# Kernel optimization log

Measured on AMD Instinct MI355X. Metric: run time of the kernel, lower is better.

The kernel has to match this reference:

```python
import jax, jax.numpy as jnp
from jax import lax
import numpy as np

B = 8192
HID = 128
FILT = 256  # stft filter length
HOP = 128
PAD = 64
NBINS = 129  # FILT//2 + 1


def setup_inputs() -> dict:
    key = jax.random.key(0)
    ks = jax.random.split(key, 16)
    def rn(k, shape, fan_in):
        return jax.random.normal(k, shape, dtype=jnp.float32) / np.sqrt(fan_in)
    inp = {
        "audio_input": jax.random.normal(ks[0], (B, 4160), dtype=jnp.float32),
        "hidden_state": jnp.zeros((B, HID), dtype=jnp.float32),
        "cell_state": jnp.zeros((B, HID), dtype=jnp.float32),
        # STFT forward basis: [2*NBINS, 1, FILT] (real then imag banks)
        "stft_w": rn(ks[1], (2 * NBINS, 1, FILT), FILT),
        # encoder: 4 conv1d layers (out, in, k), strides 1,2,2,1, pad 1
        "enc_w1": rn(ks[2], (128, 129, 3), 129 * 3), "enc_b1": jnp.zeros((128,), jnp.float32),
        "enc_w2": rn(ks[3], (64, 128, 3), 128 * 3), "enc_b2": jnp.zeros((64,), jnp.float32),
        "enc_w3": rn(ks[4], (64, 64, 3), 64 * 3),   "enc_b3": jnp.zeros((64,), jnp.float32),
        "enc_w4": rn(ks[5], (128, 64, 3), 64 * 3),  "enc_b4": jnp.zeros((128,), jnp.float32),
        # LSTMCell (PyTorch layout): gates order i,f,g,o
        "w_ih": rn(ks[6], (4 * HID, HID), HID), "w_hh": rn(ks[7], (4 * HID, HID), HID),
        "b_ih": jnp.zeros((4 * HID,), jnp.float32), "b_hh": jnp.zeros((4 * HID,), jnp.float32),
        # output head: Linear(128 -> 1) + sigmoid
        "out_w": rn(ks[8], (1, HID), HID), "out_b": jnp.zeros((1,), jnp.float32),
    }
    return inp


def _conv1d(x, w, b, stride, pad):
    # x: [N, C_in, L], w: [C_out, C_in, k]
    y = lax.conv_general_dilated(x, w, (stride,), [(pad, pad)],
                                 dimension_numbers=("NCH", "OIH", "NCH"))
    return y + b[None, :, None]


def reference(audio_input, hidden_state, cell_state, stft_w,
              enc_w1, enc_b1, enc_w2, enc_b2, enc_w3, enc_b3, enc_w4, enc_b4,
              w_ih, w_hh, b_ih, b_hh, out_w, out_b):
    b = audio_input.shape[0]
    # chunk i with context == audio_input[:, i*512 : i*512 + 576]
    chunks = jnp.stack([audio_input[:, i * 512:i * 512 + 576] for i in range(8)], axis=0)  # [8,B,576]
    x = chunks.reshape(8 * b, 576)
    # STFT: reflect pad 64 each side, conv stride 128 -> [8B, 258, 4]
    xp = jnp.pad(x, ((0, 0), (PAD, PAD)), mode="reflect")[:, None, :]
    spec = lax.conv_general_dilated(xp, stft_w, (HOP,), "VALID",
                                    dimension_numbers=("NCH", "OIH", "NCH"))
    mag = jnp.sqrt(spec[:, :NBINS] ** 2 + spec[:, NBINS:] ** 2)  # [8B,129,4]
    # encoder conv stack: 4 -> 4 -> 2 -> 1 -> 1 frames
    h1 = jax.nn.relu(_conv1d(mag, enc_w1, enc_b1, 1, 1))
    h2 = jax.nn.relu(_conv1d(h1, enc_w2, enc_b2, 2, 1))
    h3 = jax.nn.relu(_conv1d(h2, enc_w3, enc_b3, 2, 1))
    h4 = jax.nn.relu(_conv1d(h3, enc_w4, enc_b4, 1, 1))  # [8B,128,1]
    feats = h4[:, :, 0].reshape(8, b, HID)  # [8,B,128]

    def step(carry, x_t):
        h, c = carry
        gates = x_t @ w_ih.T + b_ih + h @ w_hh.T + b_hh  # [B,4H]
        i_g, f_g, g_g, o_g = jnp.split(gates, 4, axis=-1)
        c_new = jax.nn.sigmoid(f_g) * c + jax.nn.sigmoid(i_g) * jnp.tanh(g_g)
        h_new = jax.nn.sigmoid(o_g) * jnp.tanh(c_new)
        p = jax.nn.sigmoid(h_new @ out_w.T + out_b)  # [B,1]
        return (h_new, c_new), p

    (h_fin, c_fin), probs = lax.scan(step, (hidden_state, cell_state), feats)  # probs [8,B,1]
    # final = 1 - prod_i (1 - p_i), shape [B,1,1]
    final = (1.0 - jnp.prod(1.0 - probs, axis=0))[:, :, None]
    return final, h_fin, c_fin
```

## Files before the change

kernel.cpp:

```cpp
#include <hip/hip_runtime.h>
#include <hip/hip_bf16.h>
#include <math.h>

typedef __hip_bfloat16 bf16;
typedef __attribute__((ext_vector_type(4))) float f32x4;
typedef __attribute__((ext_vector_type(8))) short short8;
typedef __attribute__((ext_vector_type(4))) short short4v;

#define BATCH   8192
#define NTOT    65536
#define NT2     131072
#define NW      262144
#define HID     128

__device__ __forceinline__ float b2f(bf16 v){ return __bfloat162float(v); }
__device__ __forceinline__ bf16  f2b(float v){ return __float2bfloat16(v); }
__device__ __forceinline__ short f2bs(float v){
  bf16 b = __float2bfloat16(v);
  return *reinterpret_cast<short*>(&b);
}
__device__ __forceinline__ float sigf(float x){ return 1.0f/(1.0f+__expf(-x)); }
__device__ __forceinline__ float tanhfast(float x){
  return 1.0f - 2.0f/(__expf(2.0f*x)+1.0f);
}

__global__ __launch_bounds__(256) void k_wcvt(
    const float* __restrict__ W, bf16* __restrict__ Wb)
{
  const int idx = blockIdx.x*256 + threadIdx.x;
  if (idx < 258*256) Wb[idx] = f2b(W[idx]);
}
__global__ __launch_bounds__(256) void k_w1cvt(
    const float* __restrict__ w1, bf16* __restrict__ w1b)
{
  const int idx = blockIdx.x*256 + threadIdx.x;
  if (idx >= 61440) return;
  const int dt = idx / 20480, rem = idx % 20480;
  const int cout = rem / 160, k = rem % 160;
  const float v = (k < 129) ? w1[(cout*129 + k)*3 + dt] : 0.f;
  w1b[idx] = f2b(v);
}
__global__ __launch_bounds__(256) void k_w2cvt(
    const float* __restrict__ w2, bf16* __restrict__ w2b)
{
  const int idx = blockIdx.x*256 + threadIdx.x;
  if (idx >= 24576) return;
  const int dt = idx >> 13, cout = (idx >> 7) & 63, k = idx & 127;
  w2b[idx] = f2b(w2[(cout*128 + k)*3 + dt]);
}
__global__ __launch_bounds__(256) void k_w34cvt(
    const float* __restrict__ w3, const float* __restrict__ w4,
    bf16* __restrict__ w3e, bf16* __restrict__ w4e)
{
  const int idx = blockIdx.x*256 + threadIdx.x;
  if (idx >= 16384) return;
  if (idx < 8192){
    const int row = idx >> 7, k = idx & 127;
    const int cin = k >> 1, t = k & 1;
    w3e[idx] = f2b(w3[(row*64 + cin)*3 + 1 + t]);
  } else {
    const int i2 = idx - 8192;
    const int row = i2 >> 6, cin = i2 & 63;
    w4e[i2] = f2b(w4[(row*64 + cin)*3 + 1]);
  }
}
__global__ __launch_bounds__(256) void k_wlcvt1(
    const float* __restrict__ whh, bf16* __restrict__ wl1)
{
  const int idx = blockIdx.x*256 + threadIdx.x;
  if (idx >= 65536) return;
  wl1[idx] = f2b(whh[idx]);
}
__global__ __launch_bounds__(256) void k_wlxcvt(
    const float* __restrict__ wih, bf16* __restrict__ wlx)
{
  const int idx = blockIdx.x*256 + threadIdx.x;
  if (idx >= 65536) return;
  wlx[idx] = f2b(wih[idx]);
}

__global__ __launch_bounds__(256) void k_stft3(
    const float* __restrict__ audio, const bf16* __restrict__ Wb,
    bf16* __restrict__ mag)
{
  __shared__ __align__(16) char ALDS[96*512];
  __shared__ __align__(16) bf16 refl[4*8*64];
  const int tid = threadIdx.x, lane = tid & 63, wq = tid >> 6;
  const int r0 = blockIdx.x * 4;
  const float* arow = audio + (size_t)(r0 + wq) * 4160;

  #pragma unroll
  for (int q = 0; q < 8; ++q){
    const int e = q*64 + lane;
    const int i = e >> 6, k = e & 63;
    refl[(wq*8 + i)*64 + k] = f2b(arow[512*i + 64 - k]);
  }

  const int kgo8 = (lane>>4)*8;
  short8 Bfrag[2][8];
  #pragma unroll
  for (int ng = 0; ng < 2; ++ng){
    const int wl = ng*16 + (lane & 15);
    const int i = wl >> 2, t = wl & 3;
    #pragma unroll
    for (int ks = 0; ks < 8; ++ks){
      const int kb = ks*32 + kgo8;
      if (t == 0 && kb < 64){
        Bfrag[ng][ks] = *(const short8*)(refl + (wq*8 + i)*64 + kb);
      } else {
        const float* src = arow + 512*i + 128*t - 64 + kb;
        const float4 v0 = *(const float4*)(src);
        const float4 v1 = *(const float4*)(src + 4);
        short8 s;
        s[0]=f2bs(v0.x); s[1]=f2bs(v0.y); s[2]=f2bs(v0.z); s[3]=f2bs(v0.w);
        s[4]=f2bs(v1.x); s[5]=f2bs(v1.y); s[6]=f2bs(v1.z); s[7]=f2bs(v1.w);
        Bfrag[ng][ks] = s;
      }
    }
  }

  const int kab = (lane>>4)*16;
  for (int pass = 0; pass < 3; ++pass){
    __syncthreads();
    for (int idx = tid; idx < 96*32; idx += 256){
      const int ar = idx >> 5;
      const int cb = (idx & 31) * 16;
      const int b3 = ar >> 5, reim = (ar >> 4) & 1, bl = ar & 15;
      int bin = pass*48 + b3*16 + bl;
      if (bin > 128) bin = 128;
      const int grow = bin + reim*129;
      int off = ar*512 + cb; off ^= ((ar&7)<<4);
      *(f32x4*)(ALDS + off) = *(const f32x4*)((const char*)Wb + grow*512 + cb);
    }
    __syncthreads();

    f32x4 accRe[3][2], accIm[3][2];
    #pragma unroll
    for (int b3 = 0; b3 < 3; ++b3)
      #pragma unroll
      for (int ng = 0; ng < 2; ++ng){
        accRe[b3][ng] = f32x4{0.f,0.f,0.f,0.f};
        accIm[b3][ng] = f32x4{0.f,0.f,0.f,0.f};
      }
    #pragma unroll
    for (int ks = 0; ks < 8; ++ks){
      #pragma unroll
      for (int b3 = 0; b3 < 3; ++b3){
        const int arRe = b3*32 + (lane & 15);
        const int arIm = arRe + 16;
        int offRe = arRe*512 + ks*64 + kab; offRe ^= ((arRe&7)<<4);
        int offIm = arIm*512 + ks*64 + kab; offIm ^= ((arIm&7)<<4);
        const short8 aRe = *(const short8*)(ALDS + offRe);
        const short8 aIm = *(const short8*)(ALDS + offIm);
        #pragma unroll
        for (int ng = 0; ng < 2; ++ng){
          accRe[b3][ng] = __builtin_amdgcn_mfma_f32_16x16x32_bf16(
              aRe, Bfrag[ng][ks], accRe[b3][ng], 0, 0, 0);
          accIm[b3][ng] = __builtin_amdgcn_mfma_f32_16x16x32_bf16(
              aIm, Bfrag[ng][ks], accIm[b3][ng], 0, 0, 0);
        }
      }
    }
    #pragma unroll
    for (int b3 = 0; b3 < 3; ++b3)
      #pragma unroll
      for (int j = 0; j < 4; ++j){
        const int bin = (pass*3 + b3)*16 + (lane>>4)*4 + j;
        if (bin <= 128){
          #pragma unroll
          for (int ng = 0; ng < 2; ++ng){
            const int wl = ng*16 + (lane & 15);
            const int i = wl >> 2, t = wl & 3;
            const float re = accRe[b3][ng][j], im = accIm[b3][ng][j];
            mag[(size_t)bin*NW + (size_t)i*32768 + (r0+wq)*4 + t] =
                f2b(sqrtf(re*re + im*im));
          }
        }
      }
  }
}

#define E1_LDS (192*320)
__global__ __launch_bounds__(256) void k_enc1_gemm(
    const bf16* __restrict__ mag, const bf16* __restrict__ w1b,
    const float* __restrict__ b1, bf16* __restrict__ h1)
{
  __shared__ __align__(16) char Bs[E1_LDS];
  const int tid = threadIdx.x, lane = tid & 63, wq = tid >> 6;
  const int n0 = blockIdx.x * 32;
  const int i  = n0 >> 13, b0 = n0 & 8191;
  const size_t colbase = (size_t)i*32768 + (size_t)b0*4;

  for (int off = tid*16; off < E1_LDS; off += 256*16)
    *(f32x4*)(Bs + off) = f32x4{0.f,0.f,0.f,0.f};
  __syncthreads();
  for (int it = tid; it < 129*64; it += 256){
    const int cin = it >> 6, seg = it & 63;
    const unsigned int pair =
        *(const unsigned int*)(mag + (size_t)cin*NW + colbase + seg*2);
    #pragma unroll
    for (int q = 0; q < 2; ++q){
      const int w = seg*2 + q;
      const int row = (w>>2)*6 + (w&3) + 1;
      int off = row*320 + cin*2; off ^= ((row&7)<<4);
      *(short*)(Bs + off) = (short)((q==0) ? (pair & 0xffff) : (pair >> 16));
    }
  }
  __syncthreads();

  const int wr = wq >> 1, wc = wq & 1;
  f32x4 acc[4][4];
  #pragma unroll
  for (int mg = 0; mg < 4; ++mg)
    #pragma unroll
    for (int ng = 0; ng < 4; ++ng) acc[mg][ng] = f32x4{0.f,0.f,0.f,0.f};

  int brow[4], acol[4];
  #pragma unroll
  for (int ng = 0; ng < 4; ++ng){
    const int w = wc*64 + ng*16 + (lane & 15);
    brow[ng] = (w>>2)*6 + (w&3);
  }
  #pragma unroll
  for (int mg = 0; mg < 4; ++mg) acol[mg] = wr*64 + mg*16 + (lane & 15);
  const int kb = (lane>>4)*16;

  for (int dt = 0; dt < 3; ++dt){
    #pragma unroll
    for (int ks = 0; ks < 5; ++ks){
      short8 afr[4], bfr[4];
      #pragma unroll
      for (int mg = 0; mg < 4; ++mg)
        afr[mg] = *(const short8*)((const char*)w1b +
            ((dt*128 + acol[mg])*160 + ks*32)*2 + kb);
      #pragma unroll
      for (int ng = 0; ng < 4; ++ng){
        const int row = brow[ng] + dt;
        int off = row*320 + ks*64 + kb; off ^= ((row&7)<<4);
        bfr[ng] = *(const short8*)(Bs + off);
      }
      #pragma unroll
      for (int mg = 0; mg < 4; ++mg)
        #pragma unroll
        for (int ng = 0; ng < 4; ++ng)
          acc[mg][ng] = __builtin_amdgcn_mfma_f32_16x16x32_bf16(
              afr[mg], bfr[ng], acc[mg][ng], 0, 0, 0);
    }
  }
  #pragma unroll
  for (int mg = 0; mg < 4; ++mg)
    #pragma unroll
    for (int j = 0; j < 4; ++j){
      const int cout = wr*64 + mg*16 + (lane>>4)*4 + j;
      const float bv = b1[cout];
      #pragma unroll
      for (int ng = 0; ng < 4; ++ng){
        const int col = wc*64 + ng*16 + (lane & 15);
        float v = acc[mg][ng][j] + bv; v = v > 0.f ? v : 0.f;
        h1[(size_t)cout*NW + colbase + col] = f2b(v);
      }
    }
}

#define E2_LDS (160*256)
__global__ __launch_bounds__(256) void k_enc2_gemm(
    const bf16* __restrict__ h1, const bf16* __restrict__ w2b,
    const float* __restrict__ b2, bf16* __restrict__ h2)
{
  __shared__ __align__(16) char Bs[E2_LDS];
  const int tid = threadIdx.x, lane = tid & 63, wq = tid >> 6;
  const int n0 = blockIdx.x * 32;
  const int i  = n0 >> 13, b0 = n0 & 8191;
  const size_t colbase = (size_t)i*32768 + (size_t)b0*4;
  const size_t col2base = (size_t)i*16384 + (size_t)b0*2;

  for (int off = tid*16; off < E2_LDS; off += 256*16)
    *(f32x4*)(Bs + off) = f32x4{0.f,0.f,0.f,0.f};
  __syncthreads();
  for (int it = tid; it < 128*64; it += 256){
    const int cin = it >> 6, seg = it & 63;
    const unsigned int pair =
        *(const unsigned int*)(h1 + (size_t)cin*NW + colbase + seg*2);
    #pragma unroll
    for (int q = 0; q < 2; ++q){
      const int w = seg*2 + q;
      const int row = (w>>2)*5 + (w&3) + 1;
      int off = row*256 + cin*2; off ^= ((row&7)<<4);
      *(short*)(Bs + off) = (short)((q==0) ? (pair & 0xffff) : (pair >> 16));
    }
  }
  __syncthreads();

  const int wr = wq >> 1, wc = wq & 1;
  f32x4 acc[2][2];
  #pragma unroll
  for (int mg = 0; mg < 2; ++mg)
    #pragma unroll
    for (int ng = 0; ng < 2; ++ng) acc[mg][ng] = f32x4{0.f,0.f,0.f,0.f};

  int brow[2], acol[2];
  #pragma unroll
  for (int ng = 0; ng < 2; ++ng){
    const int wl = wc*32 + ng*16 + (lane & 15);
    brow[ng] = (wl>>1)*5 + (wl&1)*2;
  }
  #pragma unroll
  for (int mg = 0; mg < 2; ++mg) acol[mg] = wr*32 + mg*16 + (lane & 15);
  const int kb = (lane>>4)*16;

  for (int dt = 0; dt < 3; ++dt){
    #pragma unroll
    for (int ks = 0; ks < 4; ++ks){
      short8 afr[2], bfr[2];
      #pragma unroll
      for (int mg = 0; mg < 2; ++mg)
        afr[mg] = *(const short8*)((const char*)w2b +
            ((dt*64 + acol[mg])*128 + ks*32)*2 + kb);
      #pragma unroll
      for (int ng = 0; ng < 2; ++ng){
        const int row = brow[ng] + dt;
        int off = row*256 + ks*64 + kb; off ^= ((row&7)<<4);
        bfr[ng] = *(const short8*)(Bs + off);
      }
      #pragma unroll
      for (int mg = 0; mg < 2; ++mg)
        #pragma unroll
        for (int ng = 0; ng < 2; ++ng)
          acc[mg][ng] = __builtin_amdgcn_mfma_f32_16x16x32_bf16(
              afr[mg], bfr[ng], acc[mg][ng], 0, 0, 0);
    }
  }
  #pragma unroll
  for (int mg = 0; mg < 2; ++mg)
    #pragma unroll
    for (int j = 0; j < 4; ++j){
      const int cout = wr*32 + mg*16 + (lane>>4)*4 + j;
      const float bv = b2[cout];
      #pragma unroll
      for (int ng = 0; ng < 2; ++ng){
        const int col = wc*32 + ng*16 + (lane & 15);
        float v = acc[mg][ng][j] + bv; v = v > 0.f ? v : 0.f;
        h2[(size_t)cout*NT2 + col2base + col] = f2b(v);
      }
    }
}

__global__ __launch_bounds__(256) void k_enc34(
    const bf16* __restrict__ h2, const bf16* __restrict__ w3e,
    const float* __restrict__ b3, const bf16* __restrict__ w4e,
    const float* __restrict__ b4, bf16* __restrict__ h4)
{
  __shared__ __align__(16) char B1[64*256];
  __shared__ __align__(16) char B2[64*128];
  const int tid = threadIdx.x, lane = tid & 63, wq = tid >> 6;
  const int n0 = blockIdx.x * 64;

  for (int it = tid; it < 64*64; it += 256){
    const int cin = it >> 6, nl = it & 63;
    const int n = n0 + nl, i = n >> 13, b = n & 8191;
    const unsigned int pair =
        *(const unsigned int*)(h2 + (size_t)cin*NT2 + i*16384 + 2*b);
    int off = nl*256 + cin*4; off ^= ((nl&7)<<4);
    *(unsigned int*)(B1 + off) = pair;
  }
  __syncthreads();

  const int kb = (lane>>4)*16;
  f32x4 acc1[4];
  #pragma unroll
  for (int ng = 0; ng < 4; ++ng) acc1[ng] = f32x4{0.f,0.f,0.f,0.f};
  const int ar1 = wq*16 + (lane & 15);
  #pragma unroll
  for (int ks = 0; ks < 4; ++ks){
    const short8 a = *(const short8*)((const char*)w3e + (ar1*128 + ks*32)*2 + kb);
    #pragma unroll
    for (int ng = 0; ng < 4; ++ng){
      const int row = ng*16 + (lane & 15);
      int off = row*256 + ks*64 + kb; off ^= ((row&7)<<4);
      const short8 bfr = *(const short8*)(B1 + off);
      acc1[ng] = __builtin_amdgcn_mfma_f32_16x16x32_bf16(a, bfr, acc1[ng], 0, 0, 0);
    }
  }
  #pragma unroll
  for (int j = 0; j < 4; ++j){
    const int r1 = wq*16 + (lane>>4)*4 + j;
    const float bv = b3[r1];
    #pragma unroll
    for (int ng = 0; ng < 4; ++ng){
      const int col = ng*16 + (lane & 15);
      float v = acc1[ng][j] + bv; v = v > 0.f ? v : 0.f;
      int off = col*128 + r1*2; off ^= ((col&7)<<4);
      *(short*)(B2 + off) = f2bs(v);
    }
  }
  __syncthreads();

  f32x4 acc2[2][4];
  #pragma unroll
  for (int mg = 0; mg < 2; ++mg)
    #pragma unroll
    for (int ng = 0; ng < 4; ++ng) acc2[mg][ng] = f32x4{0.f,0.f,0.f,0.f};
  #pragma unroll
  for (int ks = 0; ks < 2; ++ks){
    short8 bfr[4];
    #pragma unroll
    for (int ng = 0; ng < 4; ++ng){
      const int row = ng*16 + (lane & 15);
      int off = row*128 + ks*64 + kb; off ^= ((row&7)<<4);
      bfr[ng] = *(const short8*)(B2 + off);
    }
    #pragma unroll
    for (int mg = 0; mg < 2; ++mg){
      const int ar2 = wq*32 + mg*16 + (lane & 15);
      const short8 a = *(const short8*)((const char*)w4e + (ar2*64 + ks*32)*2 + kb);
      #pragma unroll
      for (int ng = 0; ng < 4; ++ng)
        acc2[mg][ng] = __builtin_amdgcn_mfma_f32_16x16x32_bf16(a, bfr[ng], acc2[mg][ng], 0, 0, 0);
    }
  }
  #pragma unroll
  for (int mg = 0; mg < 2; ++mg)
    #pragma unroll
    for (int j = 0; j < 4; ++j){
      const int cout = wq*32 + mg*16 + (lane>>4)*4 + j;
      const float bv = b4[cout];
      #pragma unroll
      for (int ng = 0; ng < 4; ++ng){
        const int n = n0 + ng*16 + (lane & 15);
        float v = acc2[mg][ng][j] + bv; v = v > 0.f ? v : 0.f;
        h4[(size_t)cout*NTOT + n] = f2b(v);
      }
    }
}

__global__ __launch_bounds__(256) void k_init(
    const float* __restrict__ h0, const float* __restrict__ c0,
    float* __restrict__ hT0, float* __restrict__ cT)
{
  const int idx = blockIdx.x*256 + threadIdx.x;
  const int b = idx >> 7, c = idx & 127;
  hT0[c*BATCH + b] = h0[idx];
  cT [c*BATCH + b] = c0[idx];
}

__global__ __launch_bounds__(256) void k_gatex(
    const bf16* __restrict__ h4, const bf16* __restrict__ wlx,
    float* __restrict__ xg, int half)
{
  __shared__ __align__(16) char Bs[32*256];
  const int tid = threadIdx.x, lane = tid & 63, wq = tid >> 6;
  const int n0 = blockIdx.x * 32;
  const int gcol = half*32768 + n0;

  for (int it = tid; it < 128*32; it += 256){
    const int cp = it >> 5, nl = it & 31;
    const bf16 v = h4[(size_t)cp*NTOT + gcol + nl];
    int off = nl*256 + cp*2; off ^= ((nl&7)<<4);
    *(short*)(Bs + off) = *(const short*)&v;
  }
  __syncthreads();

  f32x4 acc[8][2];
  #pragma unroll
  for (int mg = 0; mg < 8; ++mg)
    #pragma unroll
    for (int ng = 0; ng < 2; ++ng) acc[mg][ng] = f32x4{0.f,0.f,0.f,0.f};

  int arow[8];
  #pragma unroll
  for (int mg = 0; mg < 8; ++mg) arow[mg] = wq*128 + mg*16 + (lane & 15);
  const int kb = (lane>>4)*16;

  #pragma unroll
  for (int ks = 0; ks < 4; ++ks){
    short8 bfr[2];
    #pragma unroll
    for (int ng = 0; ng < 2; ++ng){
      const int row = ng*16 + (lane & 15);
      int off = row*256 + ks*64 + kb; off ^= ((row&7)<<4);
      bfr[ng] = *(const short8*)(Bs + off);
    }
    #pragma unroll
    for (int mg = 0; mg < 8; ++mg){
      const short8 a = *(const short8*)((const char*)wlx +
          ((size_t)arow[mg]*128 + ks*32)*2 + kb);
      #pragma unroll
      for (int ng = 0; ng < 2; ++ng)
        acc[mg][ng] = __builtin_amdgcn_mfma_f32_16x16x32_bf16(
            a, bfr[ng], acc[mg][ng], 0, 0, 0);
    }
  }

  #pragma unroll
  for (int mg = 0; mg < 8; ++mg)
    #pragma unroll
    for (int j = 0; j < 4; ++j){
      const int row = wq*128 + mg*16 + (lane>>4)*4 + j;
      #pragma unroll
      for (int ng = 0; ng < 2; ++ng){
        const int col = n0 + ng*16 + (lane & 15);
        xg[(size_t)row*32768 + col] = acc[mg][ng][j];
      }
    }
}

__global__ __launch_bounds__(256) void k_lstm_rec(
    const float* __restrict__ xg, const bf16* __restrict__ wl1,
    const float* __restrict__ bih, const float* __restrict__ bhh,
    const float* __restrict__ hprev, float* __restrict__ hout,
    float* __restrict__ cT, int s)
{
  __shared__ __align__(16) char Bs[32*256];
  const int tid = threadIdx.x, lane = tid & 63, wq = tid >> 6;
  const int b0 = blockIdx.x * 32;

  for (int it = tid; it < 128*32; it += 256){
    const int cp = it >> 5, bl = it & 31;
    const float v = hprev[cp*BATCH + b0 + bl];
    int off = bl*256 + cp*2; off ^= ((bl&7)<<4);
    *(short*)(Bs + off) = f2bs(v);
  }
  __syncthreads();

  const int c0r = wq*32;
  f32x4 acc[4][2][2];
  #pragma unroll
  for (int g = 0; g < 4; ++g)
    #pragma unroll
    for (int h = 0; h < 2; ++h)
      #pragma unroll
      for (int ng = 0; ng < 2; ++ng) acc[g][h][ng] = f32x4{0.f,0.f,0.f,0.f};

  int arow[4][2];
  #pragma unroll
  for (int g = 0; g < 4; ++g)
    #pragma unroll
    for (int h = 0; h < 2; ++h)
      arow[g][h] = (g*128 + c0r + h*16 + (lane&15))*256 + (lane>>4)*16;

  #pragma unroll
  for (int ks = 0; ks < 4; ++ks){
    short8 bfr[2];
    #pragma unroll
    for (int ng = 0; ng < 2; ++ng){
      const int row = ng*16 + (lane & 15);
      int off = row*256 + ks*64 + (lane>>4)*16; off ^= ((row&7)<<4);
      bfr[ng] = *(const short8*)(Bs + off);
    }
    #pragma unroll
    for (int g = 0; g < 4; ++g)
      #pragma unroll
      for (int h = 0; h < 2; ++h){
        const short8 a = *(const short8*)((const char*)wl1 + arow[g][h] + ks*64);
        #pragma unroll
        for (int ng = 0; ng < 2; ++ng)
          acc[g][h][ng] = __builtin_amdgcn_mfma_f32_16x16x32_bf16(
              a, bfr[ng], acc[g][h][ng], 0, 0, 0);
      }
  }

  const size_t xcolbase = (size_t)(s & 3)*8192 + b0;
  #pragma unroll
  for (int h = 0; h < 2; ++h)
    #pragma unroll
    for (int ng = 0; ng < 2; ++ng)
      #pragma unroll
      for (int j = 0; j < 4; ++j){
        const int c = c0r + h*16 + (lane>>4)*4 + j;
        const int b = b0 + ng*16 + (lane & 15);
        const size_t xc = xcolbase + ng*16 + (lane & 15);
        const float ig = acc[0][h][ng][j] + xg[(size_t)(0*128+c)*32768 + xc] + bih[c]       + bhh[c];
        const float fg = acc[1][h][ng][j] + xg[(size_t)(1*128+c)*32768 + xc] + bih[128 + c] + bhh[128 + c];
        const float gg = acc[2][h][ng][j] + xg[(size_t)(2*128+c)*32768 + xc] + bih[256 + c] + bhh[256 + c];
        const float og = acc[3][h][ng][j] + xg[(size_t)(3*128+c)*32768 + xc] + bih[384 + c] + bhh[384 + c];
        const float cold = cT[c*BATCH + b];
        const float cn = sigf(fg)*cold + sigf(ig)*tanhfast(gg);
        const float hn = sigf(og)*tanhfast(cn);
        cT  [c*BATCH + b] = cn;
        hout[c*BATCH + b] = hn;
      }
}

__global__ __launch_bounds__(256) void k_headp(
    const float* __restrict__ hseq, const float* __restrict__ ow,
    const float* __restrict__ ob, float* __restrict__ P)
{
  const int idx = blockIdx.x*256 + threadIdx.x;
  const int s = idx >> 13, b = idx & (BATCH-1);
  const float* hp = hseq + (size_t)s*HID*BATCH;
  float acc = ob[0];
  for (int c = 0; c < 128; ++c) acc += ow[c]*hp[c*BATCH + b];
  P[s*BATCH + b] = sigf(acc);
}
__global__ __launch_bounds__(256) void k_head2(
    const float* __restrict__ P, float* __restrict__ outp)
{
  const int b = blockIdx.x*256 + threadIdx.x;
  float prod = 1.f;
  #pragma unroll
  for (int s = 0; s < 8; ++s) prod *= (1.f - P[s*BATCH + b]);
  outp[b] = 1.f - prod;
}

__global__ __launch_bounds__(256) void k_outT(
    const float* __restrict__ h7, const float* __restrict__ cT,
    float* __restrict__ out)
{
  const int idx = blockIdx.x*256 + threadIdx.x;
  const int b = idx >> 7, c = idx & 127;
  out[8192 + idx]           = h7[c*BATCH + b];
  out[8192 + 1048576 + idx] = cT[c*BATCH + b];
}

extern "C" void kernel_launch(void* const* d_in, const int* in_sizes, int n_in,
                              void* d_out, int out_size, void* d_ws, size_t ws_size,
                              hipStream_t stream)
{
  (void)in_sizes; (void)n_in; (void)out_size; (void)ws_size;
  const float* audio = (const float*)d_in[0];
  const float* h0    = (const float*)d_in[1];
  const float* c0    = (const float*)d_in[2];
  const float* stftw = (const float*)d_in[3];
  const float* w1 = (const float*)d_in[4];  const float* b1 = (const float*)d_in[5];
  const float* w2 = (const float*)d_in[6];  const float* b2 = (const float*)d_in[7];
  const float* w3 = (const float*)d_in[8];  const float* b3 = (const float*)d_in[9];
  const float* w4 = (const float*)d_in[10]; const float* b4 = (const float*)d_in[11];
  const float* wih = (const float*)d_in[12]; const float* whh = (const float*)d_in[13];
  const float* bih = (const float*)d_in[14]; const float* bhh = (const float*)d_in[15];
  const float* ow  = (const float*)d_in[16]; const float* ob  = (const float*)d_in[17];
  float* out = (float*)d_out;

  char* ws = (char*)d_ws;
  bf16*  mag  = (bf16*) (ws + 0);
  bf16*  w2b  = (bf16*) (ws + 0);
  bf16*  w3e  = (bf16*) (ws + 1048576);
  bf16*  w4e  = (bf16*) (ws + 1081344);
  bf16*  h4   = (bf16*) (ws + 8388608);
  float* xg   = (float*)(ws + 25165824);
  float* hseq = (float*)(ws + 92274688);
  float* hT0  = (float*)(ws + 125829120);
  float* cT   = (float*)(ws + 130023424);
  bf16*  h1   = (bf16*) (ws + 67633152);
  bf16*  Wbf  = (bf16*) (ws + 67633152);
  bf16*  h2   = (bf16*) (ws + 134742016);
  bf16*  w1b  = (bf16*) (ws + 134742016);
  bf16*  wl1  = (bf16*) (ws + 134742016);
  bf16*  wlx  = (bf16*) (ws + 135135232);
  float* Pbuf = (float*)(ws + 135397376);

  k_wcvt  <<<258, 256, 0, stream>>>(stftw, Wbf);
  k_w1cvt <<<240, 256, 0, stream>>>(w1, w1b);
  k_stft3<<<2048, 256, 0, stream>>>(audio, Wbf, mag);
  k_enc1_gemm<<<2048, 256, 0, stream>>>(mag, w1b, b1, h1);
  k_w2cvt <<<96, 256, 0, stream>>>(w2, w2b);
  k_w34cvt<<<64, 256, 0, stream>>>(w3, w4, w3e, w4e);
  k_enc2_gemm<<<2048, 256, 0, stream>>>(h1, w2b, b2, h2);
  k_init <<<4096, 256, 0, stream>>>(h0, c0, hT0, cT);
  k_enc34<<<1024, 256, 0, stream>>>(h2, w3e, b3, w4e, b4, h4);
  k_wlcvt1<<<256, 256, 0, stream>>>(whh, wl1);
  k_wlxcvt<<<256, 256, 0, stream>>>(wih, wlx);
  for (int half = 0; half < 2; ++half){
    k_gatex<<<1024, 256, 0, stream>>>(h4, wlx, xg, half);
    for (int q = 0; q < 4; ++q){
      const int s = half*4 + q;
      const float* hprev = (s == 0) ? hT0 : (hseq + (size_t)(s-1)*HID*BATCH);
      k_lstm_rec<<<256, 256, 0, stream>>>(xg, wl1, bih, bhh, hprev,
                                          hseq + (size_t)s*HID*BATCH, cT, s);
    }
  }
  k_headp<<<256, 256, 0, stream>>>(hseq, ow, ob, Pbuf);
  k_head2<<<32, 256, 0, stream>>>(Pbuf, out);
  k_outT<<<4096, 256, 0, stream>>>(hseq + (size_t)7*HID*BATCH, cT, out);
}
```

Baseline: 471.5 us.

## Fuse all four encoder conv layers into one LDS-resident kernel

Merges the enc1, enc2 and enc3/4 kernels into a single kernel in which each block keeps intermediate activations in shared memory. This removes the global round-trips for the h1 and h2 intermediates (h1 is about 64 MB in bf16) and two kernel launches, and the workspace layout is rearranged to match. Each block now handles 32 columns in layers 3/4 instead of 64, which halves per-block MFMA work for those layers. The fused block holds a larger live register set and reuses the shared-memory buffers across stages, which may reduce occupancy.

```diff
diff --git a/kernel.cpp b/kernel.cpp
--- a/kernel.cpp
+++ b/kernel.cpp
@@ -9,7 +9,6 @@
 
 #define BATCH   8192
 #define NTOT    65536
-#define NT2     131072
 #define NW      262144
 #define HID     128
 
@@ -181,15 +180,23 @@
 }
 
 #define E1_LDS (192*320)
-__global__ __launch_bounds__(256) void k_enc1_gemm(
-    const bf16* __restrict__ mag, const bf16* __restrict__ w1b,
-    const float* __restrict__ b1, bf16* __restrict__ h1)
+__global__ __launch_bounds__(256) void k_enc1234(
+    const bf16* __restrict__ mag,
+    const bf16* __restrict__ w1b, const float* __restrict__ b1,
+    const bf16* __restrict__ w2b, const float* __restrict__ b2,
+    const bf16* __restrict__ w3e, const float* __restrict__ b3,
+    const bf16* __restrict__ w4e, const float* __restrict__ b4,
+    bf16* __restrict__ h4)
 {
   __shared__ __align__(16) char Bs[E1_LDS];
+  char* const B3 = Bs + 40960;
+  char* const B4 = Bs + 49152;
   const int tid = threadIdx.x, lane = tid & 63, wq = tid >> 6;
   const int n0 = blockIdx.x * 32;
   const int i  = n0 >> 13, b0 = n0 & 8191;
   const size_t colbase = (size_t)i*32768 + (size_t)b0*4;
+  const int kb = (lane>>4)*16;
+  const int wr = wq >> 1, wc = wq & 1;
 
   for (int off = tid*16; off < E1_LDS; off += 256*16)
     *(f32x4*)(Bs + off) = f32x4{0.f,0.f,0.f,0.f};
@@ -208,13 +215,11 @@
   }
   __syncthreads();
 
-  const int wr = wq >> 1, wc = wq & 1;
-  f32x4 acc[4][4];
+  f32x4 acc1[4][4];
   #pragma unroll
   for (int mg = 0; mg < 4; ++mg)
     #pragma unroll
-    for (int ng = 0; ng < 4; ++ng) acc[mg][ng] = f32x4{0.f,0.f,0.f,0.f};
-
+    for (int ng = 0; ng < 4; ++ng) acc1[mg][ng] = f32x4{0.f,0.f,0.f,0.f};
   int brow[4], acol[4];
   #pragma unroll
   for (int ng = 0; ng < 4; ++ng){
@@ -223,7 +228,6 @@
   }
   #pragma unroll
   for (int mg = 0; mg < 4; ++mg) acol[mg] = wr*64 + mg*16 + (lane & 15);
-  const int kb = (lane>>4)*16;
 
   for (int dt = 0; dt < 3; ++dt){
     #pragma unroll
@@ -243,9 +247,15 @@
       for (int mg = 0; mg < 4; ++mg)
         #pragma unroll
         for (int ng = 0; ng < 4; ++ng)
-          acc[mg][ng] = __builtin_amdgcn_mfma_f32_16x16x32_bf16(
-              afr[mg], bfr[ng], acc[mg][ng], 0, 0, 0);
-    }
+          acc1[mg][ng] = __builtin_amdgcn_mfma_f32_16x16x32_bf16(
+              afr[mg], bfr[ng], acc1[mg][ng], 0, 0, 0);
+    }
+  }
+  __syncthreads();
+
+  for (int it = tid; it < 32*16; it += 256){
+    const int nloc = it >> 4, cb = (it & 15)*16;
+    *(f32x4*)(Bs + (nloc*5)*256 + cb) = f32x4{0.f,0.f,0.f,0.f};
   }
   #pragma unroll
   for (int mg = 0; mg < 4; ++mg)
@@ -255,58 +265,28 @@
       const float bv = b1[cout];
       #pragma unroll
       for (int ng = 0; ng < 4; ++ng){
-        const int col = wc*64 + ng*16 + (lane & 15);
-        float v = acc[mg][ng][j] + bv; v = v > 0.f ? v : 0.f;
-        h1[(size_t)cout*NW + colbase + col] = f2b(v);
-      }
-    }
-}
-
-#define E2_LDS (160*256)
-__global__ __launch_bounds__(256) void k_enc2_gemm(
-    const bf16* __restrict__ h1, const bf16* __restrict__ w2b,
-    const float* __restrict__ b2, bf16* __restrict__ h2)
-{
-  __shared__ __align__(16) char Bs[E2_LDS];
-  const int tid = threadIdx.x, lane = tid & 63, wq = tid >> 6;
-  const int n0 = blockIdx.x * 32;
-  const int i  = n0 >> 13, b0 = n0 & 8191;
-  const size_t colbase = (size_t)i*32768 + (size_t)b0*4;
-  const size_t col2base = (size_t)i*16384 + (size_t)b0*2;
-
-  for (int off = tid*16; off < E2_LDS; off += 256*16)
-    *(f32x4*)(Bs + off) = f32x4{0.f,0.f,0.f,0.f};
-  __syncthreads();
-  for (int it = tid; it < 128*64; it += 256){
-    const int cin = it >> 6, seg = it & 63;
-    const unsigned int pair =
-        *(const unsigned int*)(h1 + (size_t)cin*NW + colbase + seg*2);
-    #pragma unroll
-    for (int q = 0; q < 2; ++q){
-      const int w = seg*2 + q;
-      const int row = (w>>2)*5 + (w&3) + 1;
-      int off = row*256 + cin*2; off ^= ((row&7)<<4);
-      *(short*)(Bs + off) = (short)((q==0) ? (pair & 0xffff) : (pair >> 16));
-    }
-  }
-  __syncthreads();
-
-  const int wr = wq >> 1, wc = wq & 1;
-  f32x4 acc[2][2];
+        const int w = wc*64 + ng*16 + (lane & 15);
+        float v = acc1[mg][ng][j] + bv; v = v > 0.f ? v : 0.f;
+        const int row5 = (w>>2)*5 + (w&3) + 1;
+        int off = row5*256 + cout*2; off ^= ((row5&7)<<4);
+        *(short*)(Bs + off) = f2bs(v);
+      }
+    }
+  __syncthreads();
+
+  f32x4 acc2[2][2];
   #pragma unroll
   for (int mg = 0; mg < 2; ++mg)
     #pragma unroll
-    for (int ng = 0; ng < 2; ++ng) acc[mg][ng] = f32x4{0.f,0.f,0.f,0.f};
-
-  int brow[2], acol[2];
+    for (int ng = 0; ng < 2; ++ng) acc2[mg][ng] = f32x4{0.f,0.f,0.f,0.f};
+  int brow2[2], acol2[2];
   #pragma unroll
   for (int ng = 0; ng < 2; ++ng){
     const int wl = wc*32 + ng*16 + (lane & 15);
-    brow[ng] = (wl>>1)*5 + (wl&1)*2;
-  }
-  #pragma unroll
-  for (int mg = 0; mg < 2; ++mg) acol[mg] = wr*32 + mg*16 + (lane & 15);
-  const int kb = (lane>>4)*16;
+    brow2[ng] = (wl>>1)*5 + (wl&1)*2;
+  }
+  #pragma unroll
+  for (int mg = 0; mg < 2; ++mg) acol2[mg] = wr*32 + mg*16 + (lane & 15);
 
   for (int dt = 0; dt < 3; ++dt){
     #pragma unroll
@@ -315,10 +295,10 @@
       #pragma unroll
       for (int mg = 0; mg < 2; ++mg)
         afr[mg] = *(const short8*)((const char*)w2b +
-            ((dt*64 + acol[mg])*128 + ks*32)*2 + kb);
+            ((dt*64 + acol2[mg])*128 + ks*32)*2 + kb);
       #pragma unroll
       for (int ng = 0; ng < 2; ++ng){
-        const int row = brow[ng] + dt;
+        const int row = brow2[ng] + dt;
         int off = row*256 + ks*64 + kb; off ^= ((row&7)<<4);
         bfr[ng] = *(const short8*)(Bs + off);
       }
@@ -326,96 +306,79 @@
       for (int mg = 0; mg < 2; ++mg)
         #pragma unroll
         for (int ng = 0; ng < 2; ++ng)
-          acc[mg][ng] = __builtin_amdgcn_mfma_f32_16x16x32_bf16(
-              afr[mg], bfr[ng], acc[mg][ng], 0, 0, 0);
-    }
-  }
+          acc2[mg][ng] = __builtin_amdgcn_mfma_f32_16x16x32_bf16(
+              afr[mg], bfr[ng], acc2[mg][ng], 0, 0, 0);
+    }
+  }
+
   #pragma unroll
   for (int mg = 0; mg < 2; ++mg)
     #pragma unroll
     for (int j = 0; j < 4; ++j){
-      const int cout = wr*32 + mg*16 + (lane>>4)*4 + j;
-      const float bv = b2[cout];
+      const int cout2 = wr*32 + mg*16 + (lane>>4)*4 + j;
+      const float bv = b2[cout2];
       #pragma unroll
       for (int ng = 0; ng < 2; ++ng){
-        const int col = wc*32 + ng*16 + (lane & 15);
-        float v = acc[mg][ng][j] + bv; v = v > 0.f ? v : 0.f;
-        h2[(size_t)cout*NT2 + col2base + col] = f2b(v);
-      }
-    }
-}
-
-__global__ __launch_bounds__(256) void k_enc34(
-    const bf16* __restrict__ h2, const bf16* __restrict__ w3e,
-    const float* __restrict__ b3, const bf16* __restrict__ w4e,
-    const float* __restrict__ b4, bf16* __restrict__ h4)
-{
-  __shared__ __align__(16) char B1[64*256];
-  __shared__ __align__(16) char B2[64*128];
-  const int tid = threadIdx.x, lane = tid & 63, wq = tid >> 6;
-  const int n0 = blockIdx.x * 64;
-
-  for (int it = tid; it < 64*64; it += 256){
-    const int cin = it >> 6, nl = it & 63;
-    const int n = n0 + nl, i = n >> 13, b = n & 8191;
-    const unsigned int pair =
-        *(const unsigned int*)(h2 + (size_t)cin*NT2 + i*16384 + 2*b);
-    int off = nl*256 + cin*4; off ^= ((nl&7)<<4);
-    *(unsigned int*)(B1 + off) = pair;
-  }
-  __syncthreads();
-
-  const int kb = (lane>>4)*16;
-  f32x4 acc1[4];
-  #pragma unroll
-  for (int ng = 0; ng < 4; ++ng) acc1[ng] = f32x4{0.f,0.f,0.f,0.f};
+        const int wl = wc*32 + ng*16 + (lane & 15);
+        float v = acc2[mg][ng][j] + bv; v = v > 0.f ? v : 0.f;
+        const int nloc = wl >> 1, tp = wl & 1;
+        int off = nloc*256 + (cout2*2 + tp)*2; off ^= ((nloc&7)<<4);
+        *(short*)(B3 + off) = f2bs(v);
+      }
+    }
+  __syncthreads();
+
+  f32x4 acc3[2];
+  acc3[0] = f32x4{0.f,0.f,0.f,0.f};
+  acc3[1] = f32x4{0.f,0.f,0.f,0.f};
   const int ar1 = wq*16 + (lane & 15);
   #pragma unroll
   for (int ks = 0; ks < 4; ++ks){
     const short8 a = *(const short8*)((const char*)w3e + (ar1*128 + ks*32)*2 + kb);
     #pragma unroll
-    for (int ng = 0; ng < 4; ++ng){
+    for (int ng = 0; ng < 2; ++ng){
       const int row = ng*16 + (lane & 15);
       int off = row*256 + ks*64 + kb; off ^= ((row&7)<<4);
-      const short8 bfr = *(const short8*)(B1 + off);
-      acc1[ng] = __builtin_amdgcn_mfma_f32_16x16x32_bf16(a, bfr, acc1[ng], 0, 0, 0);
-    }
-  }
+      const short8 bfr = *(const short8*)(B3 + off);
+      acc3[ng] = __builtin_amdgcn_mfma_f32_16x16x32_bf16(a, bfr, acc3[ng], 0, 0, 0);
+    }
+  }
+
   #pragma unroll
   for (int j = 0; j < 4; ++j){
     const int r1 = wq*16 + (lane>>4)*4 + j;
     const float bv = b3[r1];
     #pragma unroll
-    for (int ng = 0; ng < 4; ++ng){
+    for (int ng = 0; ng < 2; ++ng){
       const int col = ng*16 + (lane & 15);
-      float v = acc1[ng][j] + bv; v = v > 0.f ? v : 0.f;
+      float v = acc3[ng][j] + bv; v = v > 0.f ? v : 0.f;
       int off = col*128 + r1*2; off ^= ((col&7)<<4);
-      *(short*)(B2 + off) = f2bs(v);
-    }
-  }
-  __syncthreads();
-
-  f32x4 acc2[2][4];
+      *(short*)(B4 + off) = f2bs(v);
+    }
+  }
+  __syncthreads();
+
+  f32x4 acc4[2][2];
   #pragma unroll
   for (int mg = 0; mg < 2; ++mg)
     #pragma unroll
-    for (int ng = 0; ng < 4; ++ng) acc2[mg][ng] = f32x4{0.f,0.f,0.f,0.f};
+    for (int ng = 0; ng < 2; ++ng) acc4[mg][ng] = f32x4{0.f,0.f,0.f,0.f};
   #pragma unroll
   for (int ks = 0; ks < 2; ++ks){
-    short8 bfr[4];
-    #pragma unroll
-    for (int ng = 0; ng < 4; ++ng){
+    short8 bfr[2];
+    #pragma unroll
+    for (int ng = 0; ng < 2; ++ng){
       const int row = ng*16 + (lane & 15);
       int off = row*128 + ks*64 + kb; off ^= ((row&7)<<4);
-      bfr[ng] = *(const short8*)(B2 + off);
+      bfr[ng] = *(const short8*)(B4 + off);
     }
     #pragma unroll
     for (int mg = 0; mg < 2; ++mg){
       const int ar2 = wq*32 + mg*16 + (lane & 15);
       const short8 a = *(const short8*)((const char*)w4e + (ar2*64 + ks*32)*2 + kb);
       #pragma unroll
-      for (int ng = 0; ng < 4; ++ng)
-        acc2[mg][ng] = __builtin_amdgcn_mfma_f32_16x16x32_bf16(a, bfr[ng], acc2[mg][ng], 0, 0, 0);
+      for (int ng = 0; ng < 2; ++ng)
+        acc4[mg][ng] = __builtin_amdgcn_mfma_f32_16x16x32_bf16(a, bfr[ng], acc4[mg][ng], 0, 0, 0);
     }
   }
   #pragma unroll
@@ -425,9 +388,9 @@
       const int cout = wq*32 + mg*16 + (lane>>4)*4 + j;
       const float bv = b4[cout];
       #pragma unroll
-      for (int ng = 0; ng < 4; ++ng){
+      for (int ng = 0; ng < 2; ++ng){
         const int n = n0 + ng*16 + (lane & 15);
-        float v = acc2[mg][ng][j] + bv; v = v > 0.f ? v : 0.f;
+        float v = acc4[mg][ng][j] + bv; v = v > 0.f ? v : 0.f;
         h4[(size_t)cout*NTOT + n] = f2b(v);
       }
     }
@@ -631,34 +594,31 @@
   float* out = (float*)d_out;
 
   char* ws = (char*)d_ws;
+  bf16*  Wbf  = (bf16*) (ws + 67633152);
+  bf16*  h4   = (bf16*) (ws + 67633152);
   bf16*  mag  = (bf16*) (ws + 0);
-  bf16*  w2b  = (bf16*) (ws + 0);
-  bf16*  w3e  = (bf16*) (ws + 1048576);
-  bf16*  w4e  = (bf16*) (ws + 1081344);
-  bf16*  h4   = (bf16*) (ws + 8388608);
-  float* xg   = (float*)(ws + 25165824);
+  float* xg   = (float*)(ws + 0);
   float* hseq = (float*)(ws + 92274688);
   float* hT0  = (float*)(ws + 125829120);
   float* cT   = (float*)(ws + 130023424);
-  bf16*  h1   = (bf16*) (ws + 67633152);
-  bf16*  Wbf  = (bf16*) (ws + 67633152);
-  bf16*  h2   = (bf16*) (ws + 134742016);
   bf16*  w1b  = (bf16*) (ws + 134742016);
-  bf16*  wl1  = (bf16*) (ws + 134742016);
-  bf16*  wlx  = (bf16*) (ws + 135135232);
+  bf16*  w2b  = (bf16*) (ws + 134864896);
+  bf16*  w3e  = (bf16*) (ws + 134914048);
+  bf16*  w4e  = (bf16*) (ws + 134930432);
+  bf16*  wl1  = (bf16*) (ws + 134946816);
+  bf16*  wlx  = (bf16*) (ws + 135077888);
   float* Pbuf = (float*)(ws + 135397376);
 
   k_wcvt  <<<258, 256, 0, stream>>>(stftw, Wbf);
   k_w1cvt <<<240, 256, 0, stream>>>(w1, w1b);
-  k_stft3<<<2048, 256, 0, stream>>>(audio, Wbf, mag);
-  k_enc1_gemm<<<2048, 256, 0, stream>>>(mag, w1b, b1, h1);
   k_w2cvt <<<96, 256, 0, stream>>>(w2, w2b);
   k_w34cvt<<<64, 256, 0, stream>>>(w3, w4, w3e, w4e);
-  k_enc2_gemm<<<2048, 256, 0, stream>>>(h1, w2b, b2, h2);
-  k_init <<<4096, 256, 0, stream>>>(h0, c0, hT0, cT);
-  k_enc34<<<1024, 256, 0, stream>>>(h2, w3e, b3, w4e, b4, h4);
   k_wlcvt1<<<256, 256, 0, stream>>>(whh, wl1);
   k_wlxcvt<<<256, 256, 0, stream>>>(wih, wlx);
+  k_init  <<<4096, 256, 0, stream>>>(h0, c0, hT0, cT);
+  k_stft3<<<2048, 256, 0, stream>>>(audio, Wbf, mag);
+  k_enc1234<<<2048, 256, 0, stream>>>(mag, w1b, b1, w2b, b2, w3e, b3,
+                                      w4e, b4, h4);
   for (int half = 0; half < 2; ++half){
     k_gatex<<<1024, 256, 0, stream>>>(h4, wlx, xg, half);
     for (int q = 0; q < 4; ++q){
```

Result: faster. 435.4 us (-7.7%).
